# Optimization experiments

Hardware: AMD Instinct MI355X
Metric: run time of the kernel (lower is better)

Reference implementation:

```python
import jax, jax.numpy as jnp
import numpy as np

DT = 1.0 / 24.0
NEARZERO = 1e-5
LENF = 72
T_STEPS, N_GRID, N_OUT = 1440, 8000, 32

PHY_NAMES = ['parBETA','parFC','parK0','parK1','parK2','parLP','parPERC','parUZL','parTT',
             'parCFMAX','parCFR','parCWH','parBETAET','parC','parRT','parAC','parF0','parFMIN','parALPHA']
PHY_BOUNDS = {'parBETA':(1.0,6.0),'parFC':(50.0,1000.0),'parK0':(0.05,0.9),'parK1':(0.01,0.5),
              'parK2':(0.001,0.2),'parLP':(0.2,1.0),'parPERC':(0.0,10.0),'parUZL':(0.0,100.0),
              'parTT':(-2.5,2.5),'parCFMAX':(0.5,10.0),'parCFR':(0.0,0.1),'parCWH':(0.0,0.2),
              'parBETAET':(0.3,5.0),'parC':(0.0,1.0),'parRT':(0.0,20.0),'parAC':(0.0,2500.0),
              'parF0':(120.0,2880.0),'parFMIN':(0.0,1.0),'parALPHA':(0.5,5.0)}
DISTR_NAMES = ['rout_a','rout_b','rout_tau']
DISTR_BOUNDS = {'rout_a':(0.0,5.0),'rout_b':(0.0,12.0),'rout_tau':(0.0,48.0)}


def _descale(raw, names, bounds):
    # raw in [0,1] -> physical range lb + raw*(ub-lb); each entry is [n_grid]
    return {n: bounds[n][0] + raw[:, i] * (bounds[n][1] - bounds[n][0]) for i, n in enumerate(names)}


def setup_inputs() -> dict:
    key = jax.random.key(0)
    ks = jax.random.split(key, 7)
    u = jax.random.uniform(ks[0], (T_STEPS, N_GRID, 3), dtype=jnp.float32)
    # prcp [0,2) mm/h, tmean [-10,20) C, pet [0,0.3) mm/h
    x_phy = jnp.stack([u[..., 0] * 2.0, u[..., 1] * 30.0 - 10.0, u[..., 2] * 0.3], axis=-1)
    ac_all = jax.random.uniform(ks[1], (N_GRID,), dtype=jnp.float32) * 2000.0        # drainage area km^2
    elev_all = jax.random.uniform(ks[2], (N_GRID,), dtype=jnp.float32) * 3000.0     # elevation m
    outlet_topo = (jax.random.uniform(ks[3], (N_OUT, N_GRID)) < 0.1).astype(jnp.float32)
    areas = jax.random.uniform(ks[4], (N_GRID,), dtype=jnp.float32) * 50.0 + 1.0    # basin area km^2
    params1 = jax.random.uniform(ks[5], (N_GRID, 19), dtype=jnp.float32)            # static phy params
    params2 = jax.random.uniform(ks[6], (N_GRID, 3), dtype=jnp.float32)             # distr routing params
    return {'x_phy': x_phy, 'ac_all': ac_all, 'elev_all': elev_all,
            'outlet_topo': outlet_topo, 'areas': areas, 'params1': params1, 'params2': params2}


def _hbv(x_phy, ac_all, elev_all, outlet_topo, areas, params1, params2):
    p = _descale(params1, PHY_NAMES, PHY_BOUNDS)
    d = _descale(params2, DISTR_NAMES, DISTR_BOUNDS)
    n = x_phy.shape[1]
    init = tuple(jnp.full((n,), 1e-3, x_phy.dtype) for _ in range(5))  # SNOWPACK, MELTWATER, SM, SUZ, SLZ
    # HBV2.0 max hourly infiltration rate, decaying with drainage area (parF0 in mm/day)
    fmax = DT * p['parF0'] * (p['parFMIN'] + (1.0 - p['parFMIN'])
                              * jnp.exp(-(ac_all / (p['parAC'] + 1.0)) ** (1.0 / p['parALPHA'])))

    def step(carry, xt):
        SP, MW, SM, SUZ, SLZ = carry
        P, Tm, PET = xt[:, 0], xt[:, 1], xt[:, 2]
        rain = jnp.where(Tm >= p['parTT'], P, 0.0)
        snow = P - rain
        SP = SP + snow
        melt = jnp.minimum(jnp.maximum(p['parCFMAX'] * DT * (Tm - p['parTT']), 0.0), SP)
        MW = MW + melt; SP = SP - melt
        refr = jnp.minimum(jnp.maximum(p['parCFR'] * p['parCFMAX'] * DT * (p['parTT'] - Tm), 0.0), MW)
        SP = SP + refr; MW = MW - refr
        tosoil = jnp.maximum(MW - p['parCWH'] * SP, 0.0)
        MW = MW - tosoil
        win = rain + tosoil
        infil = jnp.minimum(win, fmax)
        qie = win - infil                                  # infiltration-excess overland flow
        sw = jnp.clip((SM / p['parFC']) ** p['parBETA'], 0.0, 1.0)
        rech = infil * sw
        SM = SM + infil - rech
        excess = jnp.maximum(SM - p['parFC'], 0.0); SM = SM - excess
        cap = jnp.minimum(SLZ, p['parC'] * SLZ * (1.0 - jnp.minimum(SM / p['parFC'], 1.0)))
        SM = SM + cap; SLZ = SLZ - cap                      # capillary rise
        ef = jnp.clip((SM / (p['parLP'] * p['parFC'])) ** p['parBETAET'], 0.0, 1.0)
        et = jnp.minimum(PET * ef, SM)
        SM = jnp.maximum(SM - et, NEARZERO)
        SUZ = SUZ + rech + excess
        perc = jnp.minimum(SUZ, p['parPERC'] * DT); SUZ = SUZ - perc
        q0 = p['parK0'] * DT * jnp.maximum(SUZ - p['parUZL'], 0.0); SUZ = SUZ - q0
        q1 = p['parK1'] * DT * SUZ; SUZ = SUZ - q1
        SLZ = SLZ + perc
        q2 = p['parK2'] * DT * SLZ; SLZ = SLZ - q2
        return (SP, MW, SM, SUZ, SLZ), qie + q0 + q1 + q2

    _, Q = jax.lax.scan(step, init, x_phy)                 # Q: [T, n_grid] grid runoff mm/h

    # Distributed gamma unit hydrograph with per-grid lag (rout_tau + parRT), length LENF hours
    lag = d['rout_tau'] + p['parRT']                       # [n_grid]
    a = jnp.maximum(d['rout_a'], 0.01)
    b = jnp.maximum(d['rout_b'], 0.01)
    tt = jnp.arange(0.5, LENF, 1.0, dtype=x_phy.dtype)     # [LENF]
    s = tt[None, :] - lag[:, None]                          # [n_grid, LENF]
    logw = (a[:, None] - 1.0) * jnp.log(jnp.maximum(s, 1e-6)) - jnp.maximum(s, 1e-6) / b[:, None]
    w = jnp.where(s > 0.0, jnp.exp(logw), 0.0)
    w = w / (jnp.sum(w, axis=1, keepdims=True) + 1e-8)      # normalized per-grid UH [n_grid, LENF]

    # Causal per-grid (depthwise) convolution: routed[t,n] = sum_k w[n,k] * Q[t-k,n]
    lhs = Q.T[None]                                         # [1, n_grid, T]
    rhs = w[:, ::-1][:, None, :]                            # [n_grid, 1, LENF] (flip -> correlation == conv)
    routed = jax.lax.conv_general_dilated(lhs, rhs, (1,), [(LENF - 1, 0)],
                                          feature_group_count=lhs.shape[1])[0].T  # [T, n_grid]
    # Area-weighted aggregation of grid runoff to outlets
    return jnp.einsum('tn,on,n->to', routed, outlet_topo, areas)  # [T, n_out]


def reference(x_phy, ac_all, elev_all, outlet_topo, areas, params1, params2):
    return _hbv(x_phy, ac_all, elev_all, outlet_topo, areas, params1, params2)
```

## Files before the change

### kernel.cpp

```cpp
#include <hip/hip_runtime.h>

#define NG 8000
#define TS 1440
#define NOUT 32
#define LENFT 72
#define DTC (1.0f/24.0f)
#define NEARZEROC 1e-5f

__device__ __forceinline__ float fexp2(float x) {
  float r; asm("v_exp_f32 %0, %1" : "=v"(r) : "v"(x)); return r;
}
__device__ __forceinline__ float flog2(float x) {
  float r; asm("v_log_f32 %0, %1" : "=v"(r) : "v"(x)); return r;
}

typedef const void __attribute__((address_space(1))) gas_void;
typedef void __attribute__((address_space(3)))       las_void;

__global__ __launch_bounds__(256) void precompute_kernel(
    const float* __restrict__ p1, const float* __restrict__ p2,
    const float* __restrict__ ac_all,
    float* __restrict__ Cst,
    float* __restrict__ W)
{
  int n = blockIdx.x * 256 + threadIdx.x;
  if (n >= NG) return;
  const float* r = p1 + n * 19;
  float BETA   = 1.0f   + r[0]  * 5.0f;
  float FC     = 50.0f  + r[1]  * 950.0f;
  float K0     = 0.05f  + r[2]  * 0.85f;
  float K1     = 0.01f  + r[3]  * 0.49f;
  float K2     = 0.001f + r[4]  * 0.199f;
  float LP     = 0.2f   + r[5]  * 0.8f;
  float PERC   =          r[6]  * 10.0f;
  float UZL    =          r[7]  * 100.0f;
  float TT     = -2.5f  + r[8]  * 5.0f;
  float CFMAX  = 0.5f   + r[9]  * 9.5f;
  float CFR    =          r[10] * 0.1f;
  float CWH    =          r[11] * 0.2f;
  float BETAET = 0.3f   + r[12] * 4.7f;
  float Cpar   =          r[13];
  float RT     =          r[14] * 20.0f;
  float AC     =          r[15] * 2500.0f;
  float F0     = 120.0f + r[16] * 2760.0f;
  float FMIN   =          r[17];
  float ALPHA  = 0.5f   + r[18] * 4.5f;

  float ac  = ac_all[n];
  float fmx = DTC * F0 * (FMIN + (1.0f - FMIN) * expf(-powf(ac / (AC + 1.0f), 1.0f / ALPHA)));

  Cst[ 0*NG+n] = TT;            Cst[ 1*NG+n] = CFMAX * DTC;
  Cst[ 2*NG+n] = CFR*CFMAX*DTC; Cst[ 3*NG+n] = CWH;
  Cst[ 4*NG+n] = fmx;           Cst[ 5*NG+n] = 1.0f / FC;
  Cst[ 6*NG+n] = BETA;          Cst[ 7*NG+n] = FC;
  Cst[ 8*NG+n] = Cpar;          Cst[ 9*NG+n] = 1.0f / (LP * FC);
  Cst[10*NG+n] = BETAET;        Cst[11*NG+n] = PERC * DTC;
  Cst[12*NG+n] = K0 * DTC;      Cst[13*NG+n] = UZL;
  Cst[14*NG+n] = K1 * DTC;      Cst[15*NG+n] = K2 * DTC;

  float a   = fmaxf(p2[n*3+0] * 5.0f,  0.01f);
  float b   = fmaxf(p2[n*3+1] * 12.0f, 0.01f);
  float lag = p2[n*3+2] * 48.0f + RT;
  float am1 = a - 1.0f, invb = 1.0f / b;
  float sum = 0.0f;
  for (int k = 0; k < LENFT; k++) {
    float s  = (k + 0.5f) - lag;
    float sm = fmaxf(s, 1e-6f);
    float wv = (s > 0.0f) ? expf(am1 * logf(sm) - sm * invb) : 0.0f;
    sum += wv;
  }
  float inv = 1.0f / (sum + 1e-8f);
  for (int k = 0; k < LENFT; k++) {
    float s  = (k + 0.5f) - lag;
    float sm = fmaxf(s, 1e-6f);
    float wv = (s > 0.0f) ? expf(am1 * logf(sm) - sm * invb) : 0.0f;
    W[k*NG + n] = wv * inv;
  }
}

struct HbvConst {
  float TT, CFMAXDT, CFRDT, CWH, FMX, IFC, BETA, FC, C, ILF, BETAET,
        PERCDT, K0DT, UZL, K1DT, K2DT;
};

__device__ __forceinline__ void load_const(const float* __restrict__ Cst,
                                           int n, HbvConst& c) {
  c.TT    =Cst[ 0*NG+n]; c.CFMAXDT=Cst[ 1*NG+n]; c.CFRDT =Cst[ 2*NG+n];
  c.CWH   =Cst[ 3*NG+n]; c.FMX    =Cst[ 4*NG+n]; c.IFC   =Cst[ 5*NG+n];
  c.BETA  =Cst[ 6*NG+n]; c.FC     =Cst[ 7*NG+n]; c.C     =Cst[ 8*NG+n];
  c.ILF   =Cst[ 9*NG+n]; c.BETAET =Cst[10*NG+n]; c.PERCDT=Cst[11*NG+n];
  c.K0DT  =Cst[12*NG+n]; c.UZL    =Cst[13*NG+n]; c.K1DT  =Cst[14*NG+n];
  c.K2DT  =Cst[15*NG+n];
}

__device__ __forceinline__ float hbv_step(float P, float Tm, float PET,
    const HbvConst& c, float& SP, float& MW, float& SM, float& SUZ, float& SLZ)
{
  float rain = (Tm >= c.TT) ? P : 0.0f;
  float snow = P - rain;
  SP += snow;
  float dT   = Tm - c.TT;
  float melt = __builtin_amdgcn_fmed3f(0.0f, c.CFMAXDT * dT, SP);
  MW += melt; SP -= melt;
  float refr = __builtin_amdgcn_fmed3f(0.0f, c.CFRDT * (-dT), MW);
  SP += refr; MW -= refr;
  float tosoil = fmaxf(MW - c.CWH * SP, 0.0f);
  MW -= tosoil;
  float win   = rain + tosoil;
  float infil = fminf(win, c.FMX);
  float qie   = win - infil;
  float sw    = fminf(fexp2(c.BETA * flog2(SM * c.IFC)), 1.0f);
  float rech  = infil * sw;
  SM += infil - rech;
  float excess = fmaxf(SM - c.FC, 0.0f);
  SM -= excess;
  float cap = fminf(SLZ, c.C * SLZ * (1.0f - fminf(SM * c.IFC, 1.0f)));
  SM += cap; SLZ -= cap;
  float ef = fminf(fexp2(c.BETAET * flog2(SM * c.ILF)), 1.0f);
  float et = fminf(PET * ef, SM);
  SM = fmaxf(SM - et, NEARZEROC);
  SUZ += rech + excess;
  float perc = fminf(SUZ, c.PERCDT);
  SUZ -= perc;
  float q0 = c.K0DT * fmaxf(SUZ - c.UZL, 0.0f);
  SUZ -= q0;
  float q1 = c.K1DT * SUZ;
  SUZ -= q1;
  SLZ += perc;
  float q2 = c.K2DT * SLZ;
  SLZ -= q2;
  return qie + q0 + q1 + q2;
}

#define LOAD8F3(A, T0)                                                        \
  { _Pragma("unroll")                                                         \
    for (int i_ = 0; i_ < 8; i_++)                                            \
      A[i_] = *reinterpret_cast<const float3*>(                               \
                  xp + (size_t)((T0) + i_) * (NG * 3)); }

__global__ __launch_bounds__(64, 1) void scan_kernel(
    const float* __restrict__ x, const float* __restrict__ Cst,
    float* __restrict__ Q)
{
  int n = blockIdx.x * 64 + threadIdx.x;
  HbvConst c; load_const(Cst, n, c);
  float SP=1e-3f, MW=1e-3f, SM=1e-3f, SUZ=1e-3f, SLZ=1e-3f;
  const float* xp = x + (size_t)n * 3;
  float* Qp = Q + n;

  float3 bufA[8], bufB[8];
  LOAD8F3(bufA, 0);
  for (int tb = 0; tb < TS; tb += 16) {
    LOAD8F3(bufB, tb + 8);
    #pragma unroll
    for (int i = 0; i < 8; i++)
      Qp[(size_t)(tb + i) * NG] =
          hbv_step(bufA[i].x, bufA[i].y, bufA[i].z, c, SP, MW, SM, SUZ, SLZ);
    if (tb + 16 < TS) LOAD8F3(bufA, tb + 16);
    #pragma unroll
    for (int i = 0; i < 8; i++)
      Qp[(size_t)(tb + 8 + i) * NG] =
          hbv_step(bufB[i].x, bufB[i].y, bufB[i].z, c, SP, MW, SM, SUZ, SLZ);
  }
}

#define TTILE 48
#define NTILES_T 30
#define NSPLIT 25
#define SUBS 5
#define QROWS (TTILE + 71)
#define NWG (NTILES_T * NSPLIT)

__global__ __launch_bounds__(256, 2) void route_kernel(
    const float* __restrict__ Q, const float* __restrict__ W,
    const float* __restrict__ topo, const float* __restrict__ areas,
    float* __restrict__ Par)
{
  __shared__ float Qs[QROWS][64];
  __shared__ float Ws[LENFT][64];
  __shared__ float Rs[TTILE][68];

  int bid  = blockIdx.x;
  int xcd  = bid & 7, pos = bid >> 3;
  const int q = NWG / 8, r = NWG % 8;
  int wgid = ((xcd < r) ? xcd * (q + 1) : r * (q + 1) + (xcd - r) * q) + pos;
  int tile  = wgid % NTILES_T;
  int split = wgid / NTILES_T;
  int t0    = tile * TTILE;
  int tid   = threadIdx.x;
  int wid   = tid >> 6, lane = tid & 63;

  int nn = tid & 63;
  int tc = wid * 12;
  int oe = tid & 31;
  int te = (tid >> 5) * 6;

  auto stage = [&](int sub) {
    int n0 = (split * SUBS + sub) * 64;
    for (int rr = wid; rr < QROWS; rr += 4) {
      int t = t0 - 71 + rr;
      if (t >= 0)
        __builtin_amdgcn_global_load_lds(
            (gas_void*)(Q + (size_t)t * NG + n0 + lane),
            (las_void*)(&Qs[rr][0]), 4, 0, 0);
      else
        Qs[rr][lane] = 0.0f;
    }
    for (int k = wid; k < LENFT; k += 4)
      __builtin_amdgcn_global_load_lds(
          (gas_void*)(W + (size_t)k * NG + n0 + lane),
          (las_void*)(&Ws[k][0]), 4, 0, 0);
  };

  float acc_out[6] = {0.f, 0.f, 0.f, 0.f, 0.f, 0.f};

  stage(0);
  for (int sub = 0; sub < SUBS; sub++) {
    int n0 = (split * SUBS + sub) * 64;

    float4 Greg[16];
    #pragma unroll
    for (int g4 = 0; g4 < 16; g4++) {
      float4 tv = *reinterpret_cast<const float4*>(&topo[oe * NG + n0 + g4 * 4]);
      float4 av = *reinterpret_cast<const float4*>(&areas[n0 + g4 * 4]);
      Greg[g4] = make_float4(tv.x * av.x, tv.y * av.y, tv.z * av.z, tv.w * av.w);
    }

    __syncthreads();

    float acc[12];
    float qwin[12];
    #pragma unroll
    for (int i = 0; i < 12; i++) { acc[i] = 0.0f; qwin[i] = Qs[tc + i][nn]; }
    #pragma unroll
    for (int kk = 0; kk < LENFT; kk++) {
      float w = Ws[71 - kk][nn];
      #pragma unroll
      for (int i = 0; i < 12; i++) acc[i] += w * qwin[i];
      #pragma unroll
      for (int i = 0; i < 11; i++) qwin[i] = qwin[i + 1];
      if (kk < 71) qwin[11] = Qs[tc + 12 + kk][nn];
    }
    #pragma unroll
    for (int i = 0; i < 12; i++) Rs[tc + i][nn] = acc[i];
    __syncthreads();

    if (sub + 1 < SUBS) stage(sub + 1);

    #pragma unroll
    for (int g4 = 0; g4 < 16; g4++) {
      float4 g = Greg[g4];
      #pragma unroll
      for (int p = 0; p < 6; p++) {
        float4 rv = *reinterpret_cast<const float4*>(&Rs[te + p][g4 * 4]);
        acc_out[p] += rv.x * g.x + rv.y * g.y + rv.z * g.z + rv.w * g.w;
      }
    }
  }

  #pragma unroll
  for (int p = 0; p < 6; p++) {
    int tg = t0 + te + p;
    Par[(split * TS + tg) * NOUT + oe] = acc_out[p];
  }
}

__global__ __launch_bounds__(256) void reduce_kernel(
    const float* __restrict__ Par, float* __restrict__ out)
{
  int i = blockIdx.x * 256 + threadIdx.x;
  if (i < TS * NOUT) {
    float s = 0.0f;
    #pragma unroll
    for (int sp = 0; sp < NSPLIT; sp++) s += Par[sp * (TS * NOUT) + i];
    out[i] = s;
  }
}

extern "C" void kernel_launch(void* const* d_in, const int* in_sizes, int n_in,
                              void* d_out, int out_size, void* d_ws, size_t ws_size,
                              hipStream_t stream)
{
  const float* x_phy  = (const float*)d_in[0];
  const float* ac_all = (const float*)d_in[1];
  const float* topo   = (const float*)d_in[3];
  const float* areas  = (const float*)d_in[4];
  const float* p1     = (const float*)d_in[5];
  const float* p2     = (const float*)d_in[6];
  float* out = (float*)d_out;

  char* ws = (char*)d_ws;
  float* Q   = (float*)(ws);
  float* W   = (float*)(ws + 46080000);
  float* Cst = (float*)(ws + 46080000 + 2304000);
  float* Par = (float*)(ws + 46080000 + 2304000 + 512000);

  hipLaunchKernelGGL(precompute_kernel, dim3(32), dim3(256), 0, stream,
                     p1, p2, ac_all, Cst, W);
  hipLaunchKernelGGL(scan_kernel, dim3(NG / 64), dim3(64), 0, stream,
                     x_phy, Cst, Q);
  hipLaunchKernelGGL(route_kernel, dim3(NWG), dim3(256), 0, stream,
                     Q, W, topo, areas, Par);
  hipLaunchKernelGGL(reduce_kernel, dim3((TS * NOUT + 255) / 256), dim3(256), 0, stream,
                     Par, out);
}
```

Baseline: 317.8 us.

## Process two grid cells per thread in HBV scan to interleave dependency chains

The scan kernel now assigns two grid cells (n and n+4000) to each thread and advances both HBV state chains in lockstep, so the independent instruction streams can hide each other's latency. The melt/refreeze pair is merged into one clamp with a selected coefficient, and the capillary term drops an outer min. The buffers become 4-step double buffers per cell. The grid is halved to 63 single-wave blocks on a GPU with far more CUs, so it trades parallelism for ILP; the algebraic rewrites may also change rounding slightly.

After: 485.2 us. 1.53x slower.

```diff
diff --git a/kernel.cpp b/kernel.cpp
--- a/kernel.cpp
+++ b/kernel.cpp
@@ -1,6 +1,7 @@
 #include <hip/hip_runtime.h>
 
 #define NG 8000
+#define NHALF 4000
 #define TS 1440
 #define NOUT 32
 #define LENFT 72
@@ -93,74 +94,113 @@
   c.K2DT  =Cst[15*NG+n];
 }
 
-__device__ __forceinline__ float hbv_step(float P, float Tm, float PET,
-    const HbvConst& c, float& SP, float& MW, float& SM, float& SUZ, float& SLZ)
-{
-  float rain = (Tm >= c.TT) ? P : 0.0f;
-  float snow = P - rain;
-  SP += snow;
-  float dT   = Tm - c.TT;
-  float melt = __builtin_amdgcn_fmed3f(0.0f, c.CFMAXDT * dT, SP);
-  MW += melt; SP -= melt;
-  float refr = __builtin_amdgcn_fmed3f(0.0f, c.CFRDT * (-dT), MW);
-  SP += refr; MW -= refr;
-  float tosoil = fmaxf(MW - c.CWH * SP, 0.0f);
-  MW -= tosoil;
-  float win   = rain + tosoil;
-  float infil = fminf(win, c.FMX);
-  float qie   = win - infil;
-  float sw    = fminf(fexp2(c.BETA * flog2(SM * c.IFC)), 1.0f);
-  float rech  = infil * sw;
-  SM += infil - rech;
-  float excess = fmaxf(SM - c.FC, 0.0f);
-  SM -= excess;
-  float cap = fminf(SLZ, c.C * SLZ * (1.0f - fminf(SM * c.IFC, 1.0f)));
-  SM += cap; SLZ -= cap;
-  float ef = fminf(fexp2(c.BETAET * flog2(SM * c.ILF)), 1.0f);
-  float et = fminf(PET * ef, SM);
-  SM = fmaxf(SM - et, NEARZEROC);
-  SUZ += rech + excess;
-  float perc = fminf(SUZ, c.PERCDT);
-  SUZ -= perc;
-  float q0 = c.K0DT * fmaxf(SUZ - c.UZL, 0.0f);
-  SUZ -= q0;
-  float q1 = c.K1DT * SUZ;
-  SUZ -= q1;
-  SLZ += perc;
-  float q2 = c.K2DT * SLZ;
-  SLZ -= q2;
-  return qie + q0 + q1 + q2;
-}
-
-#define LOAD8F3(A, T0)                                                        \
-  { _Pragma("unroll")                                                         \
-    for (int i_ = 0; i_ < 8; i_++)                                            \
-      A[i_] = *reinterpret_cast<const float3*>(                               \
-                  xp + (size_t)((T0) + i_) * (NG * 3)); }
+__device__ __forceinline__ void hbv_step2(
+    const float3 v0, const float3 v1,
+    const HbvConst& c0, const HbvConst& c1,
+    float& SP0, float& MW0, float& SM0, float& SUZ0, float& SLZ0,
+    float& SP1, float& MW1, float& SM1, float& SUZ1, float& SLZ1,
+    float& out0, float& out1)
+{
+  bool  w0    = v0.y >= c0.TT;            bool  w1    = v1.y >= c1.TT;
+  float dT0   = v0.y - c0.TT;             float dT1   = v1.y - c1.TT;
+  float rain0 = w0 ? v0.x : 0.0f;         float rain1 = w1 ? v1.x : 0.0f;
+  SP0 += v0.x - rain0;                    SP1 += v1.x - rain1;
+  float k0    = w0 ? c0.CFMAXDT : c0.CFRDT;
+  float k1    = w1 ? c1.CFMAXDT : c1.CFRDT;
+  float tr0   = __builtin_amdgcn_fmed3f(k0 * dT0, -MW0, SP0);
+  float tr1   = __builtin_amdgcn_fmed3f(k1 * dT1, -MW1, SP1);
+  MW0 += tr0; SP0 -= tr0;                 MW1 += tr1; SP1 -= tr1;
+  float tos0  = fmaxf(MW0 - c0.CWH * SP0, 0.0f);
+  float tos1  = fmaxf(MW1 - c1.CWH * SP1, 0.0f);
+  MW0 -= tos0;                            MW1 -= tos1;
+  float win0  = rain0 + tos0;             float win1  = rain1 + tos1;
+  float inf0  = fminf(win0, c0.FMX);      float inf1  = fminf(win1, c1.FMX);
+  float qie0  = win0 - inf0;              float qie1  = win1 - inf1;
+  float l0    = flog2(SM0 * c0.IFC);      float l1    = flog2(SM1 * c1.IFC);
+  float sw0   = fminf(fexp2(c0.BETA * l0), 1.0f);
+  float sw1   = fminf(fexp2(c1.BETA * l1), 1.0f);
+  float rech0 = inf0 * sw0;               float rech1 = inf1 * sw1;
+  SM0 += inf0 - rech0;                    SM1 += inf1 - rech1;
+  float exc0  = fmaxf(SM0 - c0.FC, 0.0f); float exc1  = fmaxf(SM1 - c1.FC, 0.0f);
+  SM0 -= exc0;                            SM1 -= exc1;
+  float m0    = SM0 * c0.IFC;             float m1    = SM1 * c1.IFC;
+  float u0    = fmaxf(1.0f - m0, 0.0f);   float u1    = fmaxf(1.0f - m1, 0.0f);
+  float cap0  = c0.C * SLZ0 * u0;         float cap1  = c1.C * SLZ1 * u1;
+  SM0 += cap0; SLZ0 -= cap0;              SM1 += cap1; SLZ1 -= cap1;
+  float g0    = flog2(SM0 * c0.ILF);      float g1    = flog2(SM1 * c1.ILF);
+  float ef0   = fminf(fexp2(c0.BETAET * g0), 1.0f);
+  float ef1   = fminf(fexp2(c1.BETAET * g1), 1.0f);
+  SM0 = fmaxf(SM0 - v0.z * ef0, NEARZEROC);
+  SM1 = fmaxf(SM1 - v1.z * ef1, NEARZEROC);
+  SUZ0 += rech0 + exc0;                   SUZ1 += rech1 + exc1;
+  float p0    = fminf(SUZ0, c0.PERCDT);   float p1    = fminf(SUZ1, c1.PERCDT);
+  SUZ0 -= p0;                             SUZ1 -= p1;
+  float qa0   = c0.K0DT * fmaxf(SUZ0 - c0.UZL, 0.0f);
+  float qa1   = c1.K0DT * fmaxf(SUZ1 - c1.UZL, 0.0f);
+  SUZ0 -= qa0;                            SUZ1 -= qa1;
+  float qb0   = c0.K1DT * SUZ0;           float qb1   = c1.K1DT * SUZ1;
+  SUZ0 -= qb0;                            SUZ1 -= qb1;
+  SLZ0 += p0;                             SLZ1 += p1;
+  float qc0   = c0.K2DT * SLZ0;           float qc1   = c1.K2DT * SLZ1;
+  SLZ0 -= qc0;                            SLZ1 -= qc1;
+  out0 = qie0 + qa0 + qb0 + qc0;          out1 = qie1 + qa1 + qb1 + qc1;
+}
+
+#define LD3(p, t) (*reinterpret_cast<const float3*>((p) + (size_t)(t) * (NG * 3)))
 
 __global__ __launch_bounds__(64, 1) void scan_kernel(
     const float* __restrict__ x, const float* __restrict__ Cst,
     float* __restrict__ Q)
 {
-  int n = blockIdx.x * 64 + threadIdx.x;
-  HbvConst c; load_const(Cst, n, c);
-  float SP=1e-3f, MW=1e-3f, SM=1e-3f, SUZ=1e-3f, SLZ=1e-3f;
-  const float* xp = x + (size_t)n * 3;
-  float* Qp = Q + n;
-
-  float3 bufA[8], bufB[8];
-  LOAD8F3(bufA, 0);
-  for (int tb = 0; tb < TS; tb += 16) {
-    LOAD8F3(bufB, tb + 8);
-    #pragma unroll
-    for (int i = 0; i < 8; i++)
-      Qp[(size_t)(tb + i) * NG] =
-          hbv_step(bufA[i].x, bufA[i].y, bufA[i].z, c, SP, MW, SM, SUZ, SLZ);
-    if (tb + 16 < TS) LOAD8F3(bufA, tb + 16);
-    #pragma unroll
-    for (int i = 0; i < 8; i++)
-      Qp[(size_t)(tb + 8 + i) * NG] =
-          hbv_step(bufB[i].x, bufB[i].y, bufB[i].z, c, SP, MW, SM, SUZ, SLZ);
+  int n0 = blockIdx.x * 64 + threadIdx.x;
+  if (n0 >= NHALF) return;
+  int n1 = n0 + NHALF;
+
+  HbvConst c0, c1;
+  load_const(Cst, n0, c0);
+  load_const(Cst, n1, c1);
+
+  float SP0=1e-3f, MW0=1e-3f, SM0=1e-3f, SUZ0=1e-3f, SLZ0=1e-3f;
+  float SP1=1e-3f, MW1=1e-3f, SM1=1e-3f, SUZ1=1e-3f, SLZ1=1e-3f;
+
+  const float* xp0 = x + (size_t)n0 * 3;
+  const float* xp1 = x + (size_t)n1 * 3;
+  float* Qp0 = Q + n0;
+  float* Qp1 = Q + n1;
+
+  float3 a0[4], a1[4], b0[4], b1[4];
+  #pragma unroll
+  for (int i = 0; i < 4; i++) { a0[i] = LD3(xp0, i); a1[i] = LD3(xp1, i); }
+
+  for (int tb = 0; tb < TS; tb += 8) {
+    #pragma unroll
+    for (int i = 0; i < 4; i++) {
+      b0[i] = LD3(xp0, tb + 4 + i); b1[i] = LD3(xp1, tb + 4 + i);
+    }
+    #pragma unroll
+    for (int i = 0; i < 4; i++) {
+      float o0, o1;
+      hbv_step2(a0[i], a1[i], c0, c1,
+                SP0, MW0, SM0, SUZ0, SLZ0,
+                SP1, MW1, SM1, SUZ1, SLZ1, o0, o1);
+      Qp0[(size_t)(tb + i) * NG] = o0;
+      Qp1[(size_t)(tb + i) * NG] = o1;
+    }
+    if (tb + 8 < TS) {
+      #pragma unroll
+      for (int i = 0; i < 4; i++) {
+        a0[i] = LD3(xp0, tb + 8 + i); a1[i] = LD3(xp1, tb + 8 + i);
+      }
+    }
+    #pragma unroll
+    for (int i = 0; i < 4; i++) {
+      float o0, o1;
+      hbv_step2(b0[i], b1[i], c0, c1,
+                SP0, MW0, SM0, SUZ0, SLZ0,
+                SP1, MW1, SM1, SUZ1, SLZ1, o0, o1);
+      Qp0[(size_t)(tb + 4 + i) * NG] = o0;
+      Qp1[(size_t)(tb + 4 + i) * NG] = o1;
+    }
   }
 }
 
@@ -297,7 +337,7 @@
 
   hipLaunchKernelGGL(precompute_kernel, dim3(32), dim3(256), 0, stream,
                      p1, p2, ac_all, Cst, W);
-  hipLaunchKernelGGL(scan_kernel, dim3(NG / 64), dim3(64), 0, stream,
+  hipLaunchKernelGGL(scan_kernel, dim3((NHALF + 63) / 64), dim3(64), 0, stream,
                      x_phy, Cst, Q);
   hipLaunchKernelGGL(route_kernel, dim3(NWG), dim3(256), 0, stream,
                      Q, W, topo, areas, Par);
```
